# Kernel optimization log

Hardware: AMD Instinct MI355X
Metric: run time of the kernel (lower is better)

Reference implementation:

```python
import jax, jax.numpy as jnp
import numpy as np

N_NODES = 100000


def _gcn_layer(h, W, b, src, dst, norm, n):
    # h: [N, Fin] -> [N, Fout]; normalized scatter-add aggregation (GCNConv)
    hw = h @ W
    msg = norm[:, None] * hw[src]
    out = jax.ops.segment_sum(msg, dst, num_segments=n)
    return out + b


def setup_inputs() -> dict:
    key = jax.random.key(0)
    k = jax.random.split(key, 10)
    N, E, P, F = N_NODES, 3200000, 500000, 128
    x = jax.random.normal(k[0], (N, F), dtype=jnp.float32)
    edge_index = jax.random.randint(k[1], (2, E), 0, N, dtype=jnp.int64)
    pred_edges = jax.random.randint(k[2], (P, 2), 0, N, dtype=jnp.int64)
    # Glorot-ish init for learned params
    W1 = jax.random.normal(k[3], (F, 16), dtype=jnp.float32) / np.sqrt(F)
    b1 = jnp.zeros((16,), dtype=jnp.float32)
    W2 = jax.random.normal(k[4], (16, 8), dtype=jnp.float32) / np.sqrt(16.0)
    b2 = jnp.zeros((8,), dtype=jnp.float32)
    Wl = jax.random.normal(k[5], (8, 1), dtype=jnp.float32) / np.sqrt(8.0)
    bl = jnp.zeros((1,), dtype=jnp.float32)
    return {"x": x, "edge_index": edge_index, "pred_edges": pred_edges,
            "W1": W1, "b1": b1, "W2": W2, "b2": b2, "Wl": Wl, "bl": bl}


def reference(x, edge_index, pred_edges, W1, b1, W2, b2, Wl, bl):
    n = x.shape[0]
    # GCN norm with self-loops: A_hat = D^{-1/2}(A+I)D^{-1/2}
    loop = jnp.arange(n, dtype=edge_index.dtype)
    src = jnp.concatenate([edge_index[0], loop])
    dst = jnp.concatenate([edge_index[1], loop])
    deg = jax.ops.segment_sum(jnp.ones_like(dst, dtype=x.dtype), dst, num_segments=n)
    dinv = jnp.where(deg > 0, jax.lax.rsqrt(deg), 0.0)
    norm = dinv[src] * dinv[dst]

    h = _gcn_layer(x, W1, b1, src, dst, norm, n)   # [N, 16]
    h = _gcn_layer(h, W2, b2, src, dst, norm, n)   # [N, 8]
    z = jax.nn.sigmoid(h @ Wl + bl)                # [N, 1]
    m = z[pred_edges]                              # [P, 2, 1]
    pred = m[:, 0, 0] * m[:, 1, 0]                 # [P]
    return pred
```

## Files before the change

### kernel.cpp

```cpp
#include <hip/hip_runtime.h>
#include <hip/hip_fp16.h>
#include <math.h>

#define BSHIFT 8
#define BUCK   256
#define TILE   8192
#define CAP    12288

typedef _Float16 f16x4 __attribute__((ext_vector_type(4)));
typedef _Float16 f16x8 __attribute__((ext_vector_type(8)));
typedef float    f32x4 __attribute__((ext_vector_type(4)));


__global__ __launch_bounds__(256) void k_curinit(int* __restrict__ bcursor, int nbuk) {
    int b = blockIdx.x * 256 + threadIdx.x;
    if (b < nbuk) bcursor[b] = b * CAP;
}

__global__ __launch_bounds__(1024) void k_binscatter(const int* __restrict__ src,
                                                     const int* __restrict__ dst,
                                                     int* __restrict__ bcursor,
                                                     int* __restrict__ binned, int E, int nbuk) {
    __shared__ int hc[512];
    int t = threadIdx.x;
    int tile0 = blockIdx.x * TILE;
    int tileE = min(TILE, E - tile0);
    for (int i = t; i < nbuk; i += 1024) hc[i] = 0;
    __syncthreads();
    int d[8], s[8];
    int base = t * 8;
    if (base + 8 <= tileE) {
        const int4* d4 = (const int4*)(dst + tile0 + base);
        const int4* s4 = (const int4*)(src + tile0 + base);
        int4 da = d4[0], db = d4[1];
        int4 sa = s4[0], sb = s4[1];
        d[0] = da.x; d[1] = da.y; d[2] = da.z; d[3] = da.w;
        d[4] = db.x; d[5] = db.y; d[6] = db.z; d[7] = db.w;
        s[0] = sa.x; s[1] = sa.y; s[2] = sa.z; s[3] = sa.w;
        s[4] = sb.x; s[5] = sb.y; s[6] = sb.z; s[7] = sb.w;
    } else {
#pragma unroll
        for (int q = 0; q < 8; ++q) {
            int idx = base + q;
            if (idx < tileE) { d[q] = dst[tile0 + idx]; s[q] = src[tile0 + idx]; }
            else d[q] = -1;
        }
    }
#pragma unroll
    for (int q = 0; q < 8; ++q)
        if (d[q] >= 0) atomicAdd(&hc[d[q] >> BSHIFT], 1);
    __syncthreads();
    for (int i = t; i < nbuk; i += 1024) {
        int c = hc[i];
        hc[i] = c ? atomicAdd(&bcursor[i], c) : 0;
    }
    __syncthreads();
#pragma unroll
    for (int q = 0; q < 8; ++q) {
        if (d[q] >= 0) {
            int b = d[q] >> BSHIFT;
            int pos = atomicAdd(&hc[b], 1);
            if (pos < (b + 1) * CAP)
                binned[pos] = ((d[q] & (BUCK - 1)) << 17) | s[q];
        }
    }
}

__global__ __launch_bounds__(1024) void k_sortbucket(const int* __restrict__ bcursor,
                                                     const int* __restrict__ binned,
                                                     int* __restrict__ csr_src,
                                                     int* __restrict__ rowstart,
                                                     int* __restrict__ rowend,
                                                     float* __restrict__ dinv, int N) {
    __shared__ int cnt[BUCK];
    __shared__ int scn[BUCK];
    __shared__ int cur[BUCK];
    int b = blockIdx.x, t = threadIdx.x;
    if (t < BUCK) cnt[t] = 0;
    __syncthreads();
    int beg = b * CAP;
    int end = min(bcursor[b], beg + CAP);
    int v[12];
#pragma unroll
    for (int q = 0; q < 12; ++q) {
        int e = beg + q * 1024 + t;
        v[q] = (e < end) ? binned[e] : -1;
    }
#pragma unroll
    for (int q = 0; q < 12; ++q)
        if (v[q] >= 0) atomicAdd(&cnt[v[q] >> 17], 1);
    __syncthreads();
    if (t < BUCK) scn[t] = cnt[t];
    __syncthreads();
    for (int off = 1; off < BUCK; off <<= 1) {
        int u = (t < BUCK && t >= off) ? scn[t - off] : 0;
        __syncthreads();
        if (t < BUCK) scn[t] += u;
        __syncthreads();
    }
    if (t < BUCK) {
        int excl = scn[t] - cnt[t];
        cur[t] = excl;
        int node = b * BUCK + t;
        if (node < N) {
            rowstart[node] = beg + excl;
            rowend[node]   = beg + scn[t];
            dinv[node] = rsqrtf((float)(cnt[t] + 1));
        }
    }
    __syncthreads();
#pragma unroll
    for (int q = 0; q < 12; ++q) {
        if (v[q] >= 0) {
            int pos = atomicAdd(&cur[v[q] >> 17], 1);
            csr_src[beg + pos] = v[q] & 0x1FFFF;
        }
    }
}


__global__ __launch_bounds__(256) void k_gemm1(const float* __restrict__ x,
                                               const float* __restrict__ W1,
                                               const float* __restrict__ dinv,
                                               __half* __restrict__ hw1h, int N) {
    __shared__ _Float16 sX[64 * 136];
    __shared__ _Float16 sW[16 * 136];
    __shared__ float    sDi[64];
    __shared__ _Float16 sOut[64 * 16];
    int t = threadIdx.x;
    int row0 = blockIdx.x * 64;
    for (int e = t; e < 2048; e += 256) {
        int n = e & 15, k = e >> 4;
        sW[n * 136 + k] = (_Float16)W1[k * 16 + n];
    }
    const float4* x4 = (const float4*)x;
#pragma unroll
    for (int q = 0; q < 8; ++q) {
        int e = q * 256 + t;
        int r = e >> 5, c4 = e & 31;
        int gr = row0 + r;
        float4 v = (gr < N) ? x4[(size_t)gr * 32 + c4] : make_float4(0.f, 0.f, 0.f, 0.f);
        _Float16* p = &sX[r * 136 + c4 * 4];
        p[0] = (_Float16)v.x; p[1] = (_Float16)v.y;
        p[2] = (_Float16)v.z; p[3] = (_Float16)v.w;
    }
    if (t < 64) sDi[t] = (row0 + t < N) ? dinv[row0 + t] : 0.f;
    __syncthreads();
    int w = t >> 6, l = t & 63;
    int m = l & 15, quad = l >> 4;
    f32x4 acc = {0.f, 0.f, 0.f, 0.f};
#pragma unroll
    for (int kc = 0; kc < 4; ++kc) {
        f16x8 a = *(const f16x8*)&sX[(w * 16 + m) * 136 + kc * 32 + quad * 8];
        f16x8 b = *(const f16x8*)&sW[m * 136 + kc * 32 + quad * 8];
        acc = __builtin_amdgcn_mfma_f32_16x16x32_f16(a, b, acc, 0, 0, 0);
    }
#pragma unroll
    for (int r = 0; r < 4; ++r) {
        int nl = w * 16 + quad * 4 + r;
        sOut[nl * 16 + m] = (_Float16)(acc[r] * sDi[nl]);
    }
    __syncthreads();
    int nn = t >> 2, ch = t & 3;
    int gn = row0 + nn;
    if (gn < N)
        *(float2*)&hw1h[(size_t)gn * 16 + ch * 4] = *(float2*)&sOut[nn * 16 + ch * 4];
}

__global__ __launch_bounds__(256) void k_agg1c(const int* __restrict__ rowstart,
                                               const int* __restrict__ rowend,
                                               const int* __restrict__ csr_src,
                                               const float* __restrict__ dinv,
                                               const f16x8* __restrict__ hw1v,
                                               const float* __restrict__ W2,
                                               const float* __restrict__ b1,
                                               __half* __restrict__ hw2h, int N) {
    __shared__ float sW[128], sb[16];
    __shared__ float sh[128][17];
    __shared__ float sdi[128];
    int t = threadIdx.x;
    if (t < 128) sW[t] = W2[t];
    if (t < 16)  sb[t] = b1[t];
    __syncthreads();
    int g = t >> 1, j = t & 1;
    int i = blockIdx.x * 128 + g;
    float a[8] = {0, 0, 0, 0, 0, 0, 0, 0};
    float di = 0.f;
    if (i < N) {
        int beg = rowstart[i], end = rowend[i];
        di = dinv[i];
        int c0 = beg;
        for (; c0 + 8 <= end; c0 += 8) {
            int sidx[4];
#pragma unroll
            for (int k = 0; k < 4; ++k) sidx[k] = csr_src[c0 + j + 2 * k];
            int sv[8];
#pragma unroll
            for (int m = 0; m < 8; ++m) sv[m] = __shfl(sidx[m >> 1], m & 1, 2);
            f16x8 gv[8];
#pragma unroll
            for (int m = 0; m < 8; ++m) gv[m] = hw1v[2 * (size_t)sv[m] + j];
#pragma unroll
            for (int m = 0; m < 8; ++m)
#pragma unroll
                for (int d = 0; d < 8; ++d) a[d] += (float)gv[m][d];
        }
        for (; c0 < end; ++c0) {
            f16x8 gv = hw1v[2 * (size_t)csr_src[c0] + j];
#pragma unroll
            for (int d = 0; d < 8; ++d) a[d] += (float)gv[d];
        }
        f16x8 self = hw1v[2 * (size_t)i + j];
#pragma unroll
        for (int d = 0; d < 8; ++d)
            a[d] = di * (a[d] + (float)self[d]) + sb[8 * j + d];
    }
#pragma unroll
    for (int d = 0; d < 8; ++d) sh[g][8 * j + d] = a[d];
    if (j == 0) sdi[g] = di;
    __syncthreads();
    if (i < N) {
        int jb = j * 4;
        float o0 = 0.f, o1 = 0.f, o2 = 0.f, o3 = 0.f;
#pragma unroll
        for (int k = 0; k < 16; ++k) {
            float hv = sh[g][k];
            o0 += hv * sW[k * 8 + jb + 0];
            o1 += hv * sW[k * 8 + jb + 1];
            o2 += hv * sW[k * 8 + jb + 2];
            o3 += hv * sW[k * 8 + jb + 3];
        }
        float dd = sdi[g];
        f16x4 hout = {(_Float16)(dd * o0), (_Float16)(dd * o1),
                      (_Float16)(dd * o2), (_Float16)(dd * o3)};
        *(f16x4*)&hw2h[(size_t)i * 8 + jb] = hout;
    }
}

__global__ __launch_bounds__(256) void k_agg2c(const int* __restrict__ rowstart,
                                               const int* __restrict__ rowend,
                                               const int* __restrict__ csr_src,
                                               const float* __restrict__ dinv,
                                               const f16x4* __restrict__ hw2v,
                                               const float* __restrict__ Wl,
                                               const float* __restrict__ b2,
                                               const float* __restrict__ bl,
                                               float* __restrict__ z, int N) {
    __shared__ float sW[8], sb[8], sbl;
    int t = threadIdx.x;
    if (t < 8) { sW[t] = Wl[t]; sb[t] = b2[t]; }
    if (t == 0) sbl = bl[0];
    __syncthreads();
    int g = t >> 1, j = t & 1;
    int i = blockIdx.x * 128 + g;
    float v = 0.f;
    if (i < N) {
        int beg = rowstart[i], end = rowend[i];
        float di = dinv[i];
        float a[4] = {0, 0, 0, 0};
        int c0 = beg;
        for (; c0 + 8 <= end; c0 += 8) {
            int sidx[4];
#pragma unroll
            for (int k = 0; k < 4; ++k) sidx[k] = csr_src[c0 + j + 2 * k];
            int sv[8];
#pragma unroll
            for (int m = 0; m < 8; ++m) sv[m] = __shfl(sidx[m >> 1], m & 1, 2);
            f16x4 gv[8];
#pragma unroll
            for (int m = 0; m < 8; ++m) gv[m] = hw2v[2 * (size_t)sv[m] + j];
#pragma unroll
            for (int m = 0; m < 8; ++m)
#pragma unroll
                for (int d = 0; d < 4; ++d) a[d] += (float)gv[m][d];
        }
        for (; c0 < end; ++c0) {
            f16x4 gv = hw2v[2 * (size_t)csr_src[c0] + j];
#pragma unroll
            for (int d = 0; d < 4; ++d) a[d] += (float)gv[d];
        }
        f16x4 self = hw2v[2 * (size_t)i + j];
#pragma unroll
        for (int d = 0; d < 4; ++d) {
            float h = di * (a[d] + (float)self[d]) + sb[4 * j + d];
            v += h * sW[4 * j + d];
        }
    }
    v += __shfl_xor(v, 1);
    if (i < N && j == 0) z[i] = 1.f / (1.f + __expf(-(v + sbl)));
}

__global__ __launch_bounds__(256) void k_pred(const int2* __restrict__ pe2,
                                              const float* __restrict__ z,
                                              float* __restrict__ out, int P) {
    int p = blockIdx.x * 256 + threadIdx.x;
    if (p < P) {
        int2 e = pe2[p];
        out[p] = z[e.x] * z[e.y];
    }
}


extern "C" void kernel_launch(void* const* d_in, const int* in_sizes, int n_in,
                              void* d_out, int out_size, void* d_ws, size_t ws_size,
                              hipStream_t stream) {
    const float* x  = (const float*)d_in[0];
    const int*   ei = (const int*)d_in[1];
    const int*   pe = (const int*)d_in[2];
    const float* W1 = (const float*)d_in[3];
    const float* b1 = (const float*)d_in[4];
    const float* W2 = (const float*)d_in[5];
    const float* b2 = (const float*)d_in[6];
    const float* Wl = (const float*)d_in[7];
    const float* bl = (const float*)d_in[8];
    float* out = (float*)d_out;

    const int N = in_sizes[0] / 128;
    const int E = in_sizes[1] / 2;
    const int P = in_sizes[2] / 2;
    const int NBUK = (N + BUCK - 1) >> BSHIFT;

    const int* src = ei;
    const int* dst = ei + E;

    float*  ws   = (float*)d_ws;
    float*  dinv = ws;
    __half* hw1h = (__half*)(ws + (size_t)N);
    __half* hw2h = (__half*)(ws + (size_t)9 * N);
    float*  z    = ws + (size_t)13 * N;
    int* rowstart = (int*)(ws + (size_t)14 * N);
    int* rowend   = rowstart + N;
    int* bcursor  = rowend + N;
    int* binned   = bcursor + 512;
    int* csr_src  = binned + (size_t)NBUK * CAP;

    const int B = 256;

    k_curinit<<<(NBUK + B - 1) / B, B, 0, stream>>>(bcursor, NBUK);
    k_binscatter<<<(E + TILE - 1) / TILE, 1024, 0, stream>>>(src, dst, bcursor, binned, E, NBUK);
    k_sortbucket<<<NBUK, 1024, 0, stream>>>(bcursor, binned, csr_src, rowstart, rowend, dinv, N);
    k_gemm1<<<(N + 63) / 64, B, 0, stream>>>(x, W1, dinv, hw1h, N);
    k_agg1c<<<(N + 127) / 128, B, 0, stream>>>(rowstart, rowend, csr_src, dinv,
                                               (const f16x8*)hw1h, W2, b1, hw2h, N);
    k_agg2c<<<(N + 127) / 128, B, 0, stream>>>(rowstart, rowend, csr_src, dinv,
                                               (const f16x4*)hw2h, Wl, b2, bl, z, N);
    k_pred<<<(P + B - 1) / B, B, 0, stream>>>((const int2*)pe, z, out, P);
}
```

Baseline: 224.0 us.

## Stage binned edges in LDS and write them out coalesced per bucket

The binning kernel now does a local counting sort of each tile in shared memory. A block-wide prefix scan over the bucket counts sets local offsets, the packed payloads are placed contiguously by bucket in LDS, and a final pass writes them to global memory so that consecutive threads write consecutive addresses within a bucket. This replaces scattered global stores with mostly coalesced ones, at the cost of extra LDS use (about 48KB), a 9-step scan with many barriers, and lower occupancy. Separately, the fp16 conversion of x into shared memory now uses a single vector store instead of four scalar stores.

```diff
diff --git a/kernel.cpp b/kernel.cpp
--- a/kernel.cpp
+++ b/kernel.cpp
@@ -21,11 +21,15 @@
                                                      const int* __restrict__ dst,
                                                      int* __restrict__ bcursor,
                                                      int* __restrict__ binned, int E, int nbuk) {
-    __shared__ int hc[512];
+    __shared__ int            payload[TILE];
+    __shared__ unsigned short bid16[TILE];
+    __shared__ int cnt[512];
+    __shared__ int lstart[512];
+    __shared__ int gbase[512];
     int t = threadIdx.x;
     int tile0 = blockIdx.x * TILE;
     int tileE = min(TILE, E - tile0);
-    for (int i = t; i < nbuk; i += 1024) hc[i] = 0;
+    if (t < 512) cnt[t] = 0;
     __syncthreads();
     int d[8], s[8];
     int base = t * 8;
@@ -48,21 +52,39 @@
     }
 #pragma unroll
     for (int q = 0; q < 8; ++q)
-        if (d[q] >= 0) atomicAdd(&hc[d[q] >> BSHIFT], 1);
-    __syncthreads();
-    for (int i = t; i < nbuk; i += 1024) {
-        int c = hc[i];
-        hc[i] = c ? atomicAdd(&bcursor[i], c) : 0;
+        if (d[q] >= 0) atomicAdd(&cnt[d[q] >> BSHIFT], 1);
+    __syncthreads();
+    if (t < 512) lstart[t] = cnt[t];
+    __syncthreads();
+    for (int off = 1; off < 512; off <<= 1) {
+        int u = (t < 512 && t >= off) ? lstart[t - off] : 0;
+        __syncthreads();
+        if (t < 512) lstart[t] += u;
+        __syncthreads();
+    }
+    if (t < 512) {
+        int c = cnt[t];
+        int ex = lstart[t] - c;
+        gbase[t] = c ? atomicAdd(&bcursor[t], c) : 0;
+        lstart[t] = ex;
+        cnt[t] = ex;
     }
     __syncthreads();
 #pragma unroll
     for (int q = 0; q < 8; ++q) {
         if (d[q] >= 0) {
             int b = d[q] >> BSHIFT;
-            int pos = atomicAdd(&hc[b], 1);
-            if (pos < (b + 1) * CAP)
-                binned[pos] = ((d[q] & (BUCK - 1)) << 17) | s[q];
-        }
+            int lp = atomicAdd(&cnt[b], 1);
+            payload[lp] = ((d[q] & (BUCK - 1)) << 17) | s[q];
+            bid16[lp] = (unsigned short)b;
+        }
+    }
+    __syncthreads();
+    for (int k = t; k < tileE; k += 1024) {
+        int b = bid16[k];
+        int ga = gbase[b] + (k - lstart[b]);
+        if (ga < (b + 1) * CAP)
+            binned[ga] = payload[k];
     }
 }
 
@@ -140,9 +162,8 @@
         int r = e >> 5, c4 = e & 31;
         int gr = row0 + r;
         float4 v = (gr < N) ? x4[(size_t)gr * 32 + c4] : make_float4(0.f, 0.f, 0.f, 0.f);
-        _Float16* p = &sX[r * 136 + c4 * 4];
-        p[0] = (_Float16)v.x; p[1] = (_Float16)v.y;
-        p[2] = (_Float16)v.z; p[3] = (_Float16)v.w;
+        f16x4 hv = {(_Float16)v.x, (_Float16)v.y, (_Float16)v.z, (_Float16)v.w};
+        *(f16x4*)&sX[r * 136 + c4 * 4] = hv;
     }
     if (t < 64) sDi[t] = (row0 + t < N) ? dinv[row0 + t] : 0.f;
     __syncthreads();
```

Measured after the change: 215.7 us. 3.7% less time.
